# Performance work log

Measured on AMD Instinct MI355X. Metric: run time of the kernel, lower is better.

The kernel has to match this reference:

```python
import jax, jax.numpy as jnp
import numpy as np

TOKENS_PER_SCALE = [1, 4, 16, 64, 256]  # CLS + 2x2,4x4,8x8,16x16 patch scales = 341
TOTAL = sum(TOKENS_PER_SCALE)
NUM_HEADS = 12


def build_scale_causal_mask():
    # 0 where allowed, -inf where blocked. CLS row (scale 0) attends everywhere;
    # tokens in scale i may attend to scales j <= i (and always to CLS).
    cum = np.cumsum([0] + TOKENS_PER_SCALE)
    m = np.zeros((TOTAL, TOTAL), dtype=np.float32)
    for i in range(1, len(TOKENS_PER_SCALE)):
        for j in range(len(TOKENS_PER_SCALE)):
            if j > i:
                m[cum[i]:cum[i + 1], cum[j]:cum[j + 1]] = -np.inf
    return jnp.asarray(m)


def setup_inputs() -> dict:
    key = jax.random.key(0)
    k1, k2, k3, k4, k5 = jax.random.split(key, 5)
    B, N, D = 64, TOTAL, 768
    x = jax.random.normal(k1, (B, N, D), dtype=jnp.float32)
    qkv_w = jax.random.normal(k2, (3 * D, D), dtype=jnp.float32) * 0.02
    qkv_b = jax.random.normal(k3, (3 * D,), dtype=jnp.float32) * 0.02
    proj_w = jax.random.normal(k4, (D, D), dtype=jnp.float32) * 0.02
    proj_b = jax.random.normal(k5, (D,), dtype=jnp.float32) * 0.02
    return {"x": x, "qkv_w": qkv_w, "qkv_b": qkv_b, "proj_w": proj_w, "proj_b": proj_b}


def reference(x, qkv_w, qkv_b, proj_w, proj_b):
    B, N, D = x.shape
    H = NUM_HEADS
    hd = D // H
    scale = hd ** -0.5
    mask = build_scale_causal_mask()  # [N, N]

    qkv = jnp.einsum('bnd,ed->bne', x, qkv_w) + qkv_b  # [B, N, 3D]
    qkv = qkv.reshape(B, N, 3, H, hd)
    q = jnp.transpose(qkv[:, :, 0], (0, 2, 1, 3))  # [B, H, N, hd]
    k = jnp.transpose(qkv[:, :, 1], (0, 2, 1, 3))
    v = jnp.transpose(qkv[:, :, 2], (0, 2, 1, 3))

    attn = jnp.einsum('bhqd,bhkd->bhqk', q, k) * scale + mask  # [B, H, N, N]
    attn = jax.nn.softmax(attn, axis=-1)
    out = jnp.einsum('bhqk,bhkd->bhqd', attn, v)  # [B, H, N, hd]
    out = jnp.transpose(out, (0, 2, 1, 3)).reshape(B, N, D)
    out = jnp.einsum('bnd,ed->bne', out, proj_w) + proj_b
    return out
```

## Files before the change

### kernel.cpp

```cpp
#include <hip/hip_runtime.h>
#include <hip/hip_bf16.h>

typedef float  f32x4  __attribute__((ext_vector_type(4)));
typedef __bf16 bf16x4 __attribute__((ext_vector_type(4)));
typedef __bf16 bf16x8 __attribute__((ext_vector_type(8)));

#define B_SZ  64
#define NTOK  341
#define DM    768
#define NH    12
#define HD    64
#define MTOT  (B_SZ*NTOK)
#define MP    21888
#define EQKV  2304

#define EXP2F(x) __builtin_amdgcn_exp2f(x)

__device__ __forceinline__ void gload_lds16(const __bf16* g, void* l) {
    __builtin_amdgcn_global_load_lds(
        (const __attribute__((address_space(1))) void*)g,
        (__attribute__((address_space(3))) void*)l, 16, 0, 0);
}

__global__ void cvt3_kernel(const float* __restrict__ x,  __bf16* __restrict__ xb,
                            const float* __restrict__ wqf, __bf16* __restrict__ wq,
                            const float* __restrict__ wpf, __bf16* __restrict__ wp) {
    constexpr int N1 = MTOT * DM / 4;
    constexpr int N2 = EQKV * DM / 4;
    constexpr int N3 = DM * DM / 4;
    int i = blockIdx.x * blockDim.x + threadIdx.x;
    const int stride = gridDim.x * blockDim.x;
    for (; i < N1 + N2 + N3; i += stride) {
        const float* src; __bf16* dst; int k;
        if (i < N1)           { src = x;   dst = xb; k = i; }
        else if (i < N1 + N2) { src = wqf; dst = wq; k = i - N1; }
        else                  { src = wpf; dst = wp; k = i - N1 - N2; }
        const float4 f = ((const float4*)src)[k];
        bf16x4 v;
        v[0] = (__bf16)f.x; v[1] = (__bf16)f.y; v[2] = (__bf16)f.z; v[3] = (__bf16)f.w;
        ((bf16x4*)dst)[k] = v;
    }
}

template <int EPI, int EN, int NT>
__global__ __launch_bounds__(256) void gemm128(
    const __bf16* __restrict__ A, const __bf16* __restrict__ Bw,
    const float* __restrict__ bias,
    __bf16* __restrict__ obf, float* __restrict__ of32)
{
    __shared__ __bf16 As[2][128 * 64];
    __shared__ __bf16 Bs[2][128 * 64];

    const int tid  = threadIdx.x;
    const int lane = tid & 63;
    const int w    = tid >> 6;
    const int wm   = w >> 1, wn = w & 1;
    const int qi   = lane & 15;
    const int g    = lane >> 4;

    const int nwg = gridDim.x;
    const int bid = blockIdx.x;
    const int qq = nwg >> 3, rr = nwg & 7;
    const int xcd = bid & 7, idx = bid >> 3;
    const int wg = (xcd < rr ? xcd * (qq + 1) : rr * (qq + 1) + (xcd - rr) * qq) + idx;
    const int mtile = wg / NT;
    const int ntile = wg % NT;
    const long a_row0 = (long)mtile * 128;
    const long n0     = (long)ntile * 128;

    const int slot = lane & 7;
    const __bf16* aP[4];
    const __bf16* bP[4];
#pragma unroll
    for (int it = 0; it < 4; ++it) {
        const int lrow = it * 32 + w * 8 + (lane >> 3);
        const int scol = (slot ^ (lrow & 7)) * 8;
        aP[it] = A + (a_row0 + lrow) * DM + scol;
        const int gcol = (lrow & 64) | ((lrow & 15) << 2) | ((lrow >> 4) & 3);
        bP[it] = Bw + (n0 + gcol) * DM + scol;
    }

    const f32x4 fzero = {0.f, 0.f, 0.f, 0.f};
    f32x4 acc[4][4];
#pragma unroll
    for (int i = 0; i < 4; ++i)
#pragma unroll
        for (int j = 0; j < 4; ++j) acc[i][j] = fzero;

#define STAGE(P, K0) do { \
    _Pragma("unroll") for (int it = 0; it < 4; ++it) { \
        gload_lds16(aP[it] + (K0), (char*)(&As[P][0]) + it * 4096 + w * 1024); \
        gload_lds16(bP[it] + (K0), (char*)(&Bs[P][0]) + it * 4096 + w * 1024); \
    } } while (0)

    STAGE(0, 0);
    __syncthreads();

    int cur = 0;
    for (int k0 = 0; k0 < DM; k0 += 64) {
        if (k0 + 64 < DM) STAGE(cur ^ 1, k0 + 64);

        const __bf16* pA = &As[cur][0];
        const __bf16* pB = &Bs[cur][0];
        bf16x8 af[4][2], bfr[4][2];
#pragma unroll
        for (int i = 0; i < 4; ++i) {
            const int fr = wm * 64 + i * 16 + qi;
#pragma unroll
            for (int ks = 0; ks < 2; ++ks)
                af[i][ks] = *(const bf16x8*)(pA + fr * 64 + (((ks << 2) + g) ^ (fr & 7)) * 8);
        }
#pragma unroll
        for (int j = 0; j < 4; ++j) {
            const int frb = wn * 64 + j * 16 + qi;
#pragma unroll
            for (int ks = 0; ks < 2; ++ks)
                bfr[j][ks] = *(const bf16x8*)(pB + frb * 64 + (((ks << 2) + g) ^ (frb & 7)) * 8);
        }
#pragma unroll
        for (int ks = 0; ks < 2; ++ks)
#pragma unroll
            for (int j = 0; j < 4; ++j)
#pragma unroll
                for (int i = 0; i < 4; ++i)
                    acc[i][j] = __builtin_amdgcn_mfma_f32_16x16x32_bf16(
                        af[i][ks], bfr[j][ks], acc[i][j], 0, 0, 0);

        __syncthreads();
        cur ^= 1;
    }
#undef STAGE

    const long ge0 = n0 + wn * 64 + qi * 4;
    const float4 b4 = *(const float4*)(bias + ge0);
    const float mul = (EPI == 0 && (n0 + wn * 64) < DM) ? 0.125f * 1.44269504f : 1.f;
#pragma unroll
    for (int i = 0; i < 4; ++i) {
#pragma unroll
        for (int r = 0; r < 4; ++r) {
            const long m = a_row0 + wm * 64 + i * 16 + g * 4 + r;
            if (m < MTOT) {
                if (EPI == 0) {
                    bf16x4 pv;
                    pv[0] = (__bf16)((acc[i][0][r] + b4.x) * mul);
                    pv[1] = (__bf16)((acc[i][1][r] + b4.y) * mul);
                    pv[2] = (__bf16)((acc[i][2][r] + b4.z) * mul);
                    pv[3] = (__bf16)((acc[i][3][r] + b4.w) * mul);
                    *(bf16x4*)(obf + m * EN + ge0) = pv;
                } else {
                    float4 o;
                    o.x = acc[i][0][r] + b4.x;
                    o.y = acc[i][1][r] + b4.y;
                    o.z = acc[i][2][r] + b4.z;
                    o.w = acc[i][3][r] + b4.w;
                    *(float4*)(of32 + m * EN + ge0) = o;
                }
            }
        }
    }
}

__global__ __launch_bounds__(512) void attn_kernel(
    const __bf16* __restrict__ qkv, __bf16* __restrict__ ao)
{
    const int h = blockIdx.x;
    const int b = blockIdx.y;
    const long rowb = (long)b * NTOK;

    __shared__ char vL[64 * 768];

    const int tid  = threadIdx.x;
    const int lane = tid & 63;
    const int w    = tid >> 6;
    const int g    = lane >> 4;
    const int qi   = lane & 15;

    const __bf16* kbase = qkv + rowb * EQKV + DM + h * HD + g * 8;

    bf16x8 qf0[3], qf1[3];
    int qg[3], limit[3];
#pragma unroll
    for (int s = 0; s < 3; ++s) {
        const int gi = w + 8 * s;
        const int q  = gi * 16 + qi;
        qg[s] = q;
        const int qrow = (q > NTOK - 1) ? (NTOK - 1) : q;
        const __bf16* qsrc = qkv + (rowb + qrow) * EQKV + h * HD + g * 8;
        qf0[s] = *(const bf16x8*)(qsrc);
        qf1[s] = *(const bf16x8*)(qsrc + 32);
        limit[s] = (q == 0) ? NTOK : (q < 5 ? 5 : (q < 21 ? 21 : (q < 85 ? 85 : NTOK)));
    }

#define LOADK(BUF, J) do { \
    const int kr0_ = 32 * (J) + qi; \
    int kr1_ = kr0_ + 16; if (kr1_ > NTOK - 1) kr1_ = NTOK - 1; \
    const __bf16* k0p_ = kbase + (long)kr0_ * EQKV; \
    const __bf16* k1p_ = kbase + (long)kr1_ * EQKV; \
    BUF[0] = *(const bf16x8*)(k0p_); \
    BUF[1] = *(const bf16x8*)(k0p_ + 32); \
    BUF[2] = *(const bf16x8*)(k1p_); \
    BUF[3] = *(const bf16x8*)(k1p_ + 32); \
} while (0)

    bf16x8 kr[2][4];
    LOADK(kr[0], 0);

#pragma unroll
    for (int it = 0; it < 6; ++it) {
        const int c = it * 512 + tid;
        if (c < 2816) {
            const int n  = c >> 3;
            const int dc = (c & 7) << 3;
            bf16x8 e;
            if (n < NTOK) e = *(const bf16x8*)(qkv + (rowb + n) * EQKV + 1536 + h * HD + dc);
            else { e[0]=e[1]=e[2]=e[3]=e[4]=e[5]=e[6]=e[7] = (__bf16)0.f; }
            const int s   = ((n >> 5) << 2) | ((n >> 2) & 3);
            const int off = (((n >> 4) & 1) << 3) | ((n & 3) << 1);
            const int x   = c & 7;
#pragma unroll
            for (int i = 0; i < 8; ++i) {
                const int sp = s ^ i ^ x;
                *(__bf16*)(vL + (dc + i) * 768 + sp * 16 + off) = e[i];
            }
        }
    }
    __syncthreads();

    const f32x4 fzero = {0.f, 0.f, 0.f, 0.f};
    f32x4 oacc[3][4];
    float sum[3] = {0.f, 0.f, 0.f};
#pragma unroll
    for (int s = 0; s < 3; ++s)
#pragma unroll
        for (int db = 0; db < 4; ++db) oacc[s][db] = fzero;

    const int xd = (qi & 7) ^ ((qi >> 3) & 7);

#pragma unroll 2
    for (int j = 0; j < 11; ++j) {
        if (j + 1 < 11) LOADK(kr[(j + 1) & 1], j + 1);

        bf16x8 pf[3];
#pragma unroll
        for (int s = 0; s < 3; ++s) {
            f32x4 s0 = __builtin_amdgcn_mfma_f32_16x16x32_bf16(kr[j & 1][0], qf0[s], fzero, 0, 0, 0);
            s0 = __builtin_amdgcn_mfma_f32_16x16x32_bf16(kr[j & 1][1], qf1[s], s0, 0, 0, 0);
            f32x4 s1 = __builtin_amdgcn_mfma_f32_16x16x32_bf16(kr[j & 1][2], qf0[s], fzero, 0, 0, 0);
            s1 = __builtin_amdgcn_mfma_f32_16x16x32_bf16(kr[j & 1][3], qf1[s], s1, 0, 0, 0);
#pragma unroll
            for (int r = 0; r < 4; ++r) {
                const int k0i = 32 * j + g * 4 + r;
                const float p0 = (k0i < limit[s]) ? EXP2F(s0[r]) : 0.f;
                sum[s] += p0; pf[s][r] = (__bf16)p0;
                const int k1i = k0i + 16;
                const float p1 = (k1i < limit[s]) ? EXP2F(s1[r]) : 0.f;
                sum[s] += p1; pf[s][4 + r] = (__bf16)p1;
            }
        }

#pragma unroll
        for (int db = 0; db < 4; ++db) {
            const int d  = db * 16 + qi;
            const int sp = (4 * j + g) ^ xd ^ ((2 * db) & 7);
            const bf16x8 vf = *(const bf16x8*)(vL + d * 768 + sp * 16);
#pragma unroll
            for (int s = 0; s < 3; ++s)
                oacc[s][db] = __builtin_amdgcn_mfma_f32_16x16x32_bf16(
                    vf, pf[s], oacc[s][db], 0, 0, 0);
        }
    }
#undef LOADK

#pragma unroll
    for (int s = 0; s < 3; ++s) {
        float t = sum[s];
        t += __shfl_xor(t, 16);
        t += __shfl_xor(t, 32);
        const float rinv = 1.f / t;
        if (qg[s] < NTOK) {
            const long orow = (rowb + qg[s]) * DM + h * HD;
#pragma unroll
            for (int db = 0; db < 4; ++db) {
                bf16x4 pv;
#pragma unroll
                for (int r = 0; r < 4; ++r) pv[r] = (__bf16)(oacc[s][db][r] * rinv);
                *(bf16x4*)(ao + orow + db * 16 + g * 4) = pv;
            }
        }
    }
}

extern "C" void kernel_launch(void* const* d_in, const int* in_sizes, int n_in,
                              void* d_out, int out_size, void* d_ws, size_t ws_size,
                              hipStream_t stream) {
    const float* x      = (const float*)d_in[0];
    const float* qkv_w  = (const float*)d_in[1];
    const float* qkv_b  = (const float*)d_in[2];
    const float* proj_w = (const float*)d_in[3];
    const float* proj_b = (const float*)d_in[4];
    float* out = (float*)d_out;

    char* ws = (char*)d_ws;
    constexpr size_t XB_BYTES  = (size_t)MP * DM * 2;
    constexpr size_t WQ_OFF    = XB_BYTES;
    constexpr size_t WP_OFF    = WQ_OFF + (size_t)EQKV * DM * 2;
    constexpr size_t QKV_OFF   = WP_OFF + (size_t)DM * DM * 2;

    __bf16* xb  = (__bf16*)(ws);
    __bf16* wq  = (__bf16*)(ws + WQ_OFF);
    __bf16* wp  = (__bf16*)(ws + WP_OFF);
    __bf16* qkv = (__bf16*)(ws + QKV_OFF);

    cvt3_kernel<<<2048, 256, 0, stream>>>(x, xb, qkv_w, wq, proj_w, wp);

    gemm128<0, EQKV, 18><<<171 * 18, 256, 0, stream>>>(xb, wq, qkv_b, qkv, nullptr);
    attn_kernel<<<dim3(NH, B_SZ), 512, 0, stream>>>(qkv, xb);
    gemm128<1, DM, 6><<<171 * 6, 256, 0, stream>>>(xb, wp, proj_b, nullptr, out);
}
```

Before: 224.8 us.

## Fuse fp32-to-bf16 conversion of x into the QKV GEMM A-tile staging

```diff
diff --git a/kernel.cpp b/kernel.cpp
--- a/kernel.cpp
+++ b/kernel.cpp
@@ -22,19 +22,16 @@
         (__attribute__((address_space(3))) void*)l, 16, 0, 0);
 }
 
-__global__ void cvt3_kernel(const float* __restrict__ x,  __bf16* __restrict__ xb,
-                            const float* __restrict__ wqf, __bf16* __restrict__ wq,
+__global__ void cvt2_kernel(const float* __restrict__ wqf, __bf16* __restrict__ wq,
                             const float* __restrict__ wpf, __bf16* __restrict__ wp) {
-    constexpr int N1 = MTOT * DM / 4;
     constexpr int N2 = EQKV * DM / 4;
     constexpr int N3 = DM * DM / 4;
     int i = blockIdx.x * blockDim.x + threadIdx.x;
     const int stride = gridDim.x * blockDim.x;
-    for (; i < N1 + N2 + N3; i += stride) {
+    for (; i < N2 + N3; i += stride) {
         const float* src; __bf16* dst; int k;
-        if (i < N1)           { src = x;   dst = xb; k = i; }
-        else if (i < N1 + N2) { src = wqf; dst = wq; k = i - N1; }
-        else                  { src = wpf; dst = wp; k = i - N1 - N2; }
+        if (i < N2) { src = wqf; dst = wq; k = i; }
+        else        { src = wpf; dst = wp; k = i - N2; }
         const float4 f = ((const float4*)src)[k];
         bf16x4 v;
         v[0] = (__bf16)f.x; v[1] = (__bf16)f.y; v[2] = (__bf16)f.z; v[3] = (__bf16)f.w;
@@ -42,9 +39,9 @@
     }
 }
 
-template <int EPI, int EN, int NT>
+template <int EPI, int EN, int NT, int ACVT>
 __global__ __launch_bounds__(256) void gemm128(
-    const __bf16* __restrict__ A, const __bf16* __restrict__ Bw,
+    const void* __restrict__ Araw, const __bf16* __restrict__ Bw,
     const float* __restrict__ bias,
     __bf16* __restrict__ obf, float* __restrict__ of32)
 {
@@ -69,13 +66,17 @@
     const long n0     = (long)ntile * 128;
 
     const int slot = lane & 7;
-    const __bf16* aP[4];
+    const float*  aPf[4];
+    const __bf16* aPb[4];
     const __bf16* bP[4];
 #pragma unroll
     for (int it = 0; it < 4; ++it) {
         const int lrow = it * 32 + w * 8 + (lane >> 3);
         const int scol = (slot ^ (lrow & 7)) * 8;
-        aP[it] = A + (a_row0 + lrow) * DM + scol;
+        long arow = a_row0 + lrow;
+        if (ACVT && arow > MTOT - 1) arow = MTOT - 1;
+        aPf[it] = (const float*)Araw  + arow * DM + scol;
+        aPb[it] = (const __bf16*)Araw + arow * DM + scol;
         const int gcol = (lrow & 64) | ((lrow & 15) << 2) | ((lrow >> 4) & 3);
         bP[it] = Bw + (n0 + gcol) * DM + scol;
     }
@@ -87,18 +88,46 @@
 #pragma unroll
         for (int j = 0; j < 4; ++j) acc[i][j] = fzero;
 
-#define STAGE(P, K0) do { \
+    float4 anext[4][2];
+
+#define STAGE_B(P, K0) do { \
+    _Pragma("unroll") for (int it = 0; it < 4; ++it) \
+        gload_lds16(bP[it] + (K0), (char*)(&Bs[P][0]) + it * 4096 + w * 1024); \
+    } while (0)
+
+#define STAGE_A_GLD(P, K0) do { \
+    _Pragma("unroll") for (int it = 0; it < 4; ++it) \
+        gload_lds16(aPb[it] + (K0), (char*)(&As[P][0]) + it * 4096 + w * 1024); \
+    } while (0)
+
+#define STAGE_A_LOAD(K0) do { \
     _Pragma("unroll") for (int it = 0; it < 4; ++it) { \
-        gload_lds16(aP[it] + (K0), (char*)(&As[P][0]) + it * 4096 + w * 1024); \
-        gload_lds16(bP[it] + (K0), (char*)(&Bs[P][0]) + it * 4096 + w * 1024); \
+        anext[it][0] = *(const float4*)(aPf[it] + (K0)); \
+        anext[it][1] = *(const float4*)(aPf[it] + (K0) + 4); \
     } } while (0)
 
-    STAGE(0, 0);
+#define STAGE_A_WRITE(P) do { \
+    _Pragma("unroll") for (int it = 0; it < 4; ++it) { \
+        bf16x8 v_; \
+        v_[0] = (__bf16)anext[it][0].x; v_[1] = (__bf16)anext[it][0].y; \
+        v_[2] = (__bf16)anext[it][0].z; v_[3] = (__bf16)anext[it][0].w; \
+        v_[4] = (__bf16)anext[it][1].x; v_[5] = (__bf16)anext[it][1].y; \
+        v_[6] = (__bf16)anext[it][1].z; v_[7] = (__bf16)anext[it][1].w; \
+        *(bf16x8*)((char*)(&As[P][0]) + it * 4096 + w * 1024 + lane * 16) = v_; \
+    } } while (0)
+
+    if (ACVT) { STAGE_A_LOAD(0); STAGE_B(0, 0); STAGE_A_WRITE(0); }
+    else      { STAGE_A_GLD(0, 0); STAGE_B(0, 0); }
     __syncthreads();
 
     int cur = 0;
     for (int k0 = 0; k0 < DM; k0 += 64) {
-        if (k0 + 64 < DM) STAGE(cur ^ 1, k0 + 64);
+        const bool more = (k0 + 64 < DM);
+        if (more) {
+            if (ACVT) STAGE_A_LOAD(k0 + 64);
+            else      STAGE_A_GLD(cur ^ 1, k0 + 64);
+            STAGE_B(cur ^ 1, k0 + 64);
+        }
 
         const __bf16* pA = &As[cur][0];
         const __bf16* pB = &Bs[cur][0];
@@ -126,10 +155,14 @@
                     acc[i][j] = __builtin_amdgcn_mfma_f32_16x16x32_bf16(
                         af[i][ks], bfr[j][ks], acc[i][j], 0, 0, 0);
 
+        if (ACVT && more) STAGE_A_WRITE(cur ^ 1);
         __syncthreads();
         cur ^= 1;
     }
-#undef STAGE
+#undef STAGE_B
+#undef STAGE_A_GLD
+#undef STAGE_A_LOAD
+#undef STAGE_A_WRITE
 
     const long ge0 = n0 + wn * 64 + qi * 4;
     const float4 b4 = *(const float4*)(bias + ge0);
@@ -160,7 +193,7 @@
     }
 }
 
-__global__ __launch_bounds__(512) void attn_kernel(
+__global__ __launch_bounds__(512, 4) void attn_kernel(
     const __bf16* __restrict__ qkv, __bf16* __restrict__ ao)
 {
     const int h = blockIdx.x;
@@ -306,14 +339,14 @@
     constexpr size_t WP_OFF    = WQ_OFF + (size_t)EQKV * DM * 2;
     constexpr size_t QKV_OFF   = WP_OFF + (size_t)DM * DM * 2;
 
-    __bf16* xb  = (__bf16*)(ws);
+    __bf16* ao  = (__bf16*)(ws);
     __bf16* wq  = (__bf16*)(ws + WQ_OFF);
     __bf16* wp  = (__bf16*)(ws + WP_OFF);
     __bf16* qkv = (__bf16*)(ws + QKV_OFF);
 
-    cvt3_kernel<<<2048, 256, 0, stream>>>(x, xb, qkv_w, wq, proj_w, wp);
-
-    gemm128<0, EQKV, 18><<<171 * 18, 256, 0, stream>>>(xb, wq, qkv_b, qkv, nullptr);
-    attn_kernel<<<dim3(NH, B_SZ), 512, 0, stream>>>(qkv, xb);
-    gemm128<1, DM, 6><<<171 * 6, 256, 0, stream>>>(xb, wp, proj_b, nullptr, out);
-}
+    cvt2_kernel<<<576, 256, 0, stream>>>(qkv_w, wq, proj_w, wp);
+
+    gemm128<0, EQKV, 18, 1><<<171 * 18, 256, 0, stream>>>(x, wq, qkv_b, qkv, nullptr);
+    attn_kernel<<<dim3(NH, B_SZ), 512, 0, stream>>>(qkv, ao);
+    gemm128<1, DM, 6, 0><<<171 * 6, 256, 0, stream>>>(ao, wp, proj_b, nullptr, out);
+}
```

After: 462.5 us. 106% more time.
